# Performance work log

Measured on AMD Instinct MI355X. Metric: run time of the kernel, lower is better.

Reference implementation:

```python
import jax, jax.numpy as jnp
import numpy as np

D_K = 64

def setup_inputs() -> dict:
    key = jax.random.key(0)
    kq, kk, kv = jax.random.split(key, 3)
    B, Lq, Lk, d = 32, 2048, 2048, D_K
    return {
        "query": jax.random.normal(kq, (B, Lq, d), dtype=jnp.float32),
        "key": jax.random.normal(kk, (B, Lk, d), dtype=jnp.float32),
        "value": jax.random.normal(kv, (B, Lk, d), dtype=jnp.float32),
    }

def reference(query, key, value):
    d_k = query.shape[-1]
    scale = 1.0 / jnp.sqrt(jnp.asarray(d_k, query.dtype))
    scores = jnp.einsum('nqd,nkd->nqk', query, key) * scale  # (B, Lq, Lk)
    attn = jax.nn.softmax(scores, axis=-1)  # masked=None -> plain softmax; dropout p=0.0 is identity
    return jnp.einsum('nqk,nkd->nqd', attn, value)  # (B, Lq, d_v)
```

## Files before the change

### kernel.cpp

```cpp
#include <hip/hip_runtime.h>


#define NB   32
#define LSEQ 2048
#define DH   64
#define BM   128
#define BN   64
#define NIT  (LSEQ / BN)
#define LDP  72

typedef __attribute__((ext_vector_type(8))) __bf16 bf16x8;
typedef __attribute__((ext_vector_type(4))) float f32x4;

union BF8 { bf16x8 v; unsigned short u[8]; };

__device__ __forceinline__ unsigned short f2bf(float f) {
    unsigned int u = __builtin_bit_cast(unsigned int, f);
    u += 0x7fffu + ((u >> 16) & 1u);
    return (unsigned short)(u >> 16);
}

__device__ __forceinline__ float fast_exp2(float x) {
#if __has_builtin(__builtin_amdgcn_exp2f)
    return __builtin_amdgcn_exp2f(x);
#else
    return exp2f(x);
#endif
}

__device__ __forceinline__ void load_lds16(const void* g, void* l) {
    __builtin_amdgcn_global_load_lds(
        (const __attribute__((address_space(1))) void*)g,
        (__attribute__((address_space(3))) void*)l, 16, 0, 0);
}

__global__ __launch_bounds__(256)
void prep_k(const float* __restrict__ Kg, unsigned short* __restrict__ Kb) {
    const int CH = blockIdx.x * 256 + threadIdx.x;
    const int b   = CH >> 14;
    const int rem = CH & 16383;
    const int n   = rem >> 3;
    const int cc  = rem & 7;
    const int c   = cc ^ (n & 7);
    const float* src = Kg + (((size_t)b * LSEQ + n) * DH + c * 8);
    float4 f0 = ((const float4*)src)[0];
    float4 f1 = ((const float4*)src)[1];
    BF8 t;
    t.u[0]=f2bf(f0.x); t.u[1]=f2bf(f0.y); t.u[2]=f2bf(f0.z); t.u[3]=f2bf(f0.w);
    t.u[4]=f2bf(f1.x); t.u[5]=f2bf(f1.y); t.u[6]=f2bf(f1.z); t.u[7]=f2bf(f1.w);
    *(bf16x8*)&Kb[(size_t)CH * 8] = t.v;
}

__global__ __launch_bounds__(256)
void prep_v(const float* __restrict__ Vg, unsigned short* __restrict__ Vt) {
    __shared__ unsigned short T[64 * 65];
    const int tid = threadIdx.x;
    const int b  = blockIdx.y;
    const int nt = blockIdx.x;
    const int nl = tid >> 2;
    const int dc = (tid & 3) * 16;
    const float* src = Vg + (((size_t)b * LSEQ + nt * 64 + nl) * DH + dc);
    float4 f0 = ((const float4*)src)[0];
    float4 f1 = ((const float4*)src)[1];
    float4 f2 = ((const float4*)src)[2];
    float4 f3 = ((const float4*)src)[3];
    float vv[16] = {f0.x,f0.y,f0.z,f0.w, f1.x,f1.y,f1.z,f1.w,
                    f2.x,f2.y,f2.z,f2.w, f3.x,f3.y,f3.z,f3.w};
    #pragma unroll
    for (int i = 0; i < 16; ++i)
        T[(dc + i) * 65 + nl] = f2bf(vv[i]);
    __syncthreads();
    #pragma unroll
    for (int i = 0; i < 2; ++i) {
        const int CH = i * 256 + tid;
        const int d  = CH >> 3;
        const int cc = CH & 7;
        const int nloc = (cc ^ (d & 7)) * 8;
        BF8 o;
        #pragma unroll
        for (int j = 0; j < 8; ++j) o.u[j] = T[d * 65 + nloc + j];
        *(bf16x8*)&Vt[(((size_t)(b * 64 + d)) * 256 + nt * 8 + cc) * 8] = o.v;
    }
}

__global__ __launch_bounds__(256, 2)
void attn_fwd(const unsigned short* __restrict__ Kb,
              const unsigned short* __restrict__ Vt,
              const float* __restrict__ Qg,
              float* __restrict__ Og) {
    __shared__ __align__(16) unsigned short Klds[BN * DH];
    __shared__ __align__(16) unsigned short Vlds[DH * BN];
    __shared__ __align__(16) unsigned short Plds[4 * 32 * LDP];

    const int tid  = threadIdx.x;
    const int wave = tid >> 6;
    const int lane = tid & 63;
    const int quad = lane >> 4;
    const int l16  = lane & 15;
    const int b    = blockIdx.y;
    const int qt   = blockIdx.x;

    int fidx[4][2];
    #pragma unroll
    for (int t = 0; t < 4; ++t)
        #pragma unroll
        for (int kt = 0; kt < 2; ++kt) {
            const int n = t * 16 + l16;
            const int c = kt * 4 + quad;
            fidx[t][kt] = (n * 8 + (c ^ (n & 7))) * 8;
        }

    const float qscale = 0.18033688011112042f;
    bf16x8 qf[2][2];
    #pragma unroll
    for (int st = 0; st < 2; ++st) {
        const int row = qt * BM + wave * 32 + st * 16 + l16;
        const float* qp = Qg + (((size_t)b * LSEQ + row) * DH);
        #pragma unroll
        for (int kt = 0; kt < 2; ++kt) {
            const float* p4 = qp + kt * 32 + quad * 8;
            float4 f0 = ((const float4*)p4)[0];
            float4 f1 = ((const float4*)p4)[1];
            BF8 t;
            t.u[0]=f2bf(f0.x*qscale); t.u[1]=f2bf(f0.y*qscale);
            t.u[2]=f2bf(f0.z*qscale); t.u[3]=f2bf(f0.w*qscale);
            t.u[4]=f2bf(f1.x*qscale); t.u[5]=f2bf(f1.y*qscale);
            t.u[6]=f2bf(f1.z*qscale); t.u[7]=f2bf(f1.w*qscale);
            qf[st][kt] = t.v;
        }
    }

    f32x4 o[2][4];
    float l_run[2][4];
    #pragma unroll
    for (int st = 0; st < 2; ++st)
        #pragma unroll
        for (int t = 0; t < 4; ++t) {
            o[st][t] = (f32x4){0.f, 0.f, 0.f, 0.f};
            l_run[st][t] = 0.f;
        }

    const char* kgb = (const char*)Kb + (size_t)b * (LSEQ * DH * 2);
    const char* vgb = (const char*)Vt + (size_t)b * (DH * LSEQ * 2);
    const int L0 = wave * 128 + lane;
    const int L1 = L0 + 64;
    const int voff0 = (L0 >> 3) * (LSEQ * 2) + (L0 & 7) * 16;
    const int voff1 = (L1 >> 3) * (LSEQ * 2) + (L1 & 7) * 16;
    char* kl = (char*)Klds + wave * 2048;
    char* vl = (char*)Vlds + wave * 2048;
    unsigned short* pw = &Plds[wave * 32 * LDP];

    for (int nt = 0; nt < NIT; ++nt) {
        __syncthreads();
        load_lds16(kgb + nt * 8192 + L0 * 16, kl);
        load_lds16(kgb + nt * 8192 + L1 * 16, kl + 1024);
        load_lds16(vgb + nt * 128 + voff0, vl);
        load_lds16(vgb + nt * 128 + voff1, vl + 1024);
        __syncthreads();

        f32x4 s[2][4];
        #pragma unroll
        for (int st = 0; st < 2; ++st)
            #pragma unroll
            for (int t = 0; t < 4; ++t) s[st][t] = (f32x4){0.f, 0.f, 0.f, 0.f};
        #pragma unroll
        for (int kt = 0; kt < 2; ++kt)
            #pragma unroll
            for (int t = 0; t < 4; ++t) {
                bf16x8 kf = *(const bf16x8*)&Klds[fidx[t][kt]];
                s[0][t] = __builtin_amdgcn_mfma_f32_16x16x32_bf16(qf[0][kt], kf, s[0][t], 0, 0, 0);
                s[1][t] = __builtin_amdgcn_mfma_f32_16x16x32_bf16(qf[1][kt], kf, s[1][t], 0, 0, 0);
            }

        #pragma unroll
        for (int st = 0; st < 2; ++st)
            #pragma unroll
            for (int t = 0; t < 4; ++t)
                #pragma unroll
                for (int r = 0; r < 4; ++r) {
                    float e = fast_exp2(s[st][t][r]);
                    l_run[st][r] += e;
                    pw[(st * 16 + quad * 4 + r) * LDP + t * 16 + l16] = f2bf(e);
                }
        asm volatile("s_waitcnt lgkmcnt(0)" ::: "memory");

        #pragma unroll
        for (int kt = 0; kt < 2; ++kt) {
            bf16x8 pa0 = *(const bf16x8*)&pw[l16 * LDP + kt * 32 + quad * 8];
            bf16x8 pa1 = *(const bf16x8*)&pw[(16 + l16) * LDP + kt * 32 + quad * 8];
            #pragma unroll
            for (int t = 0; t < 4; ++t) {
                bf16x8 vf = *(const bf16x8*)&Vlds[fidx[t][kt]];
                o[0][t] = __builtin_amdgcn_mfma_f32_16x16x32_bf16(pa0, vf, o[0][t], 0, 0, 0);
                o[1][t] = __builtin_amdgcn_mfma_f32_16x16x32_bf16(pa1, vf, o[1][t], 0, 0, 0);
            }
        }
    }

    #pragma unroll
    for (int st = 0; st < 2; ++st)
        #pragma unroll
        for (int r = 0; r < 4; ++r) {
            float l = l_run[st][r];
            l += __shfl_xor(l, 1, 64);
            l += __shfl_xor(l, 2, 64);
            l += __shfl_xor(l, 4, 64);
            l += __shfl_xor(l, 8, 64);
            const float inv = 1.0f / l;
            const int row = qt * BM + wave * 32 + st * 16 + quad * 4 + r;
            float* op = Og + (((size_t)b * LSEQ + row) * DH);
            #pragma unroll
            for (int t = 0; t < 4; ++t)
                op[t * 16 + l16] = o[st][t][r] * inv;
        }
}

extern "C" void kernel_launch(void* const* d_in, const int* in_sizes, int n_in,
                              void* d_out, int out_size, void* d_ws, size_t ws_size,
                              hipStream_t stream) {
    const float* Q = (const float*)d_in[0];
    const float* K = (const float*)d_in[1];
    const float* V = (const float*)d_in[2];
    float* O = (float*)d_out;

    unsigned short* Kb = (unsigned short*)d_ws;
    unsigned short* Vt = (unsigned short*)d_ws + 4u * 1024u * 1024u;

    prep_k<<<dim3((NB * LSEQ * 8) / 256), dim3(256), 0, stream>>>(K, Kb);
    prep_v<<<dim3(LSEQ / 64, NB), dim3(256), 0, stream>>>(V, Vt);
    attn_fwd<<<dim3(LSEQ / BM, NB), dim3(256), 0, stream>>>(Kb, Vt, Q, O);
}
```

Measured before the change: 152.8 us.

## Switch attention to 32x32x16 MFMA, double-buffer K/V LDS, merge prep kernels

Replaces the 16x16x32 MFMA tiling with 32x32x16 MFMA computing S^T = K·Q^T, so each lane owns one query row and the row-sum needs only one cross-half shuffle. K/V tiles are double-buffered in LDS so the next tile's global->LDS load overlaps current compute, removing one barrier per iteration. The K and V conversion kernels are merged into one launch, and P is packed into bf16 pairs with a perm and written and read as 64-bit LDS accesses. The output is stored as float4, and the P row stride changes to 68. This uses more LDS for the double buffers and may affect occupancy. The bf16 rounding in pack_bf2 is a simplified round-half-up rather than round-to-nearest-even.

```diff
diff --git a/kernel.cpp b/kernel.cpp
--- a/kernel.cpp
+++ b/kernel.cpp
@@ -7,17 +7,23 @@
 #define BM   128
 #define BN   64
 #define NIT  (LSEQ / BN)
-#define LDP  72
-
-typedef __attribute__((ext_vector_type(8))) __bf16 bf16x8;
-typedef __attribute__((ext_vector_type(4))) float f32x4;
-
-union BF8 { bf16x8 v; unsigned short u[8]; };
+#define LDP  68
+
+typedef __attribute__((ext_vector_type(8)))  __bf16 bf16x8;
+typedef __attribute__((ext_vector_type(16))) float  f32x16;
+
+union BF8 { bf16x8 v; unsigned short u[8]; unsigned long long q[2]; };
 
 __device__ __forceinline__ unsigned short f2bf(float f) {
     unsigned int u = __builtin_bit_cast(unsigned int, f);
     u += 0x7fffu + ((u >> 16) & 1u);
     return (unsigned short)(u >> 16);
+}
+
+__device__ __forceinline__ unsigned pack_bf2(float a, float b) {
+    unsigned ua = __builtin_bit_cast(unsigned, a) + 0x8000u;
+    unsigned ub = __builtin_bit_cast(unsigned, b) + 0x8000u;
+    return __builtin_amdgcn_perm(ub, ua, 0x07060302u);
 }
 
 __device__ __forceinline__ float fast_exp2(float x) {
@@ -34,52 +40,54 @@
         (__attribute__((address_space(3))) void*)l, 16, 0, 0);
 }
 
+#define KPREP_BLOCKS ((NB * LSEQ * 8) / 256)
 __global__ __launch_bounds__(256)
-void prep_k(const float* __restrict__ Kg, unsigned short* __restrict__ Kb) {
-    const int CH = blockIdx.x * 256 + threadIdx.x;
-    const int b   = CH >> 14;
-    const int rem = CH & 16383;
-    const int n   = rem >> 3;
-    const int cc  = rem & 7;
-    const int c   = cc ^ (n & 7);
-    const float* src = Kg + (((size_t)b * LSEQ + n) * DH + c * 8);
-    float4 f0 = ((const float4*)src)[0];
-    float4 f1 = ((const float4*)src)[1];
-    BF8 t;
-    t.u[0]=f2bf(f0.x); t.u[1]=f2bf(f0.y); t.u[2]=f2bf(f0.z); t.u[3]=f2bf(f0.w);
-    t.u[4]=f2bf(f1.x); t.u[5]=f2bf(f1.y); t.u[6]=f2bf(f1.z); t.u[7]=f2bf(f1.w);
-    *(bf16x8*)&Kb[(size_t)CH * 8] = t.v;
-}
-
-__global__ __launch_bounds__(256)
-void prep_v(const float* __restrict__ Vg, unsigned short* __restrict__ Vt) {
+void prep(const float* __restrict__ Kg, const float* __restrict__ Vg,
+          unsigned short* __restrict__ Kb, unsigned short* __restrict__ Vt) {
     __shared__ unsigned short T[64 * 65];
     const int tid = threadIdx.x;
-    const int b  = blockIdx.y;
-    const int nt = blockIdx.x;
-    const int nl = tid >> 2;
-    const int dc = (tid & 3) * 16;
-    const float* src = Vg + (((size_t)b * LSEQ + nt * 64 + nl) * DH + dc);
-    float4 f0 = ((const float4*)src)[0];
-    float4 f1 = ((const float4*)src)[1];
-    float4 f2 = ((const float4*)src)[2];
-    float4 f3 = ((const float4*)src)[3];
-    float vv[16] = {f0.x,f0.y,f0.z,f0.w, f1.x,f1.y,f1.z,f1.w,
-                    f2.x,f2.y,f2.z,f2.w, f3.x,f3.y,f3.z,f3.w};
-    #pragma unroll
-    for (int i = 0; i < 16; ++i)
-        T[(dc + i) * 65 + nl] = f2bf(vv[i]);
-    __syncthreads();
-    #pragma unroll
-    for (int i = 0; i < 2; ++i) {
-        const int CH = i * 256 + tid;
-        const int d  = CH >> 3;
-        const int cc = CH & 7;
-        const int nloc = (cc ^ (d & 7)) * 8;
-        BF8 o;
-        #pragma unroll
-        for (int j = 0; j < 8; ++j) o.u[j] = T[d * 65 + nloc + j];
-        *(bf16x8*)&Vt[(((size_t)(b * 64 + d)) * 256 + nt * 8 + cc) * 8] = o.v;
+    if (blockIdx.x < KPREP_BLOCKS) {
+        const int CH  = blockIdx.x * 256 + tid;
+        const int b   = CH >> 14;
+        const int rem = CH & 16383;
+        const int n   = rem >> 3;
+        const int cc  = rem & 7;
+        const int c   = cc ^ (n & 7);
+        const float* src = Kg + (((size_t)b * LSEQ + n) * DH + c * 8);
+        float4 f0 = ((const float4*)src)[0];
+        float4 f1 = ((const float4*)src)[1];
+        BF8 t;
+        t.u[0]=f2bf(f0.x); t.u[1]=f2bf(f0.y); t.u[2]=f2bf(f0.z); t.u[3]=f2bf(f0.w);
+        t.u[4]=f2bf(f1.x); t.u[5]=f2bf(f1.y); t.u[6]=f2bf(f1.z); t.u[7]=f2bf(f1.w);
+        *(bf16x8*)&Kb[(size_t)CH * 8] = t.v;
+    } else {
+        const int bx = blockIdx.x - KPREP_BLOCKS;
+        const int b  = bx >> 5;
+        const int nt = bx & 31;
+        const int nl = tid >> 2;
+        const int dc = (tid & 3) * 16;
+        const float* src = Vg + (((size_t)b * LSEQ + nt * 64 + nl) * DH + dc);
+        float4 f0 = ((const float4*)src)[0];
+        float4 f1 = ((const float4*)src)[1];
+        float4 f2 = ((const float4*)src)[2];
+        float4 f3 = ((const float4*)src)[3];
+        float vv[16] = {f0.x,f0.y,f0.z,f0.w, f1.x,f1.y,f1.z,f1.w,
+                        f2.x,f2.y,f2.z,f2.w, f3.x,f3.y,f3.z,f3.w};
+        #pragma unroll
+        for (int i = 0; i < 16; ++i)
+            T[(dc + i) * 65 + nl] = f2bf(vv[i]);
+        __syncthreads();
+        #pragma unroll
+        for (int i = 0; i < 2; ++i) {
+            const int CH = i * 256 + tid;
+            const int d  = CH >> 3;
+            const int cc = CH & 7;
+            const int nloc = (cc ^ (d & 7)) * 8;
+            BF8 o;
+            #pragma unroll
+            for (int j = 0; j < 8; ++j) o.u[j] = T[d * 65 + nloc + j];
+            *(bf16x8*)&Vt[(((size_t)(b * 64 + d)) * 256 + nt * 8 + cc) * 8] = o.v;
+        }
     }
 }
 
@@ -88,37 +96,33 @@
               const unsigned short* __restrict__ Vt,
               const float* __restrict__ Qg,
               float* __restrict__ Og) {
-    __shared__ __align__(16) unsigned short Klds[BN * DH];
-    __shared__ __align__(16) unsigned short Vlds[DH * BN];
+    __shared__ __align__(16) unsigned short Klds[2][BN * DH];
+    __shared__ __align__(16) unsigned short Vlds[2][DH * BN];
     __shared__ __align__(16) unsigned short Plds[4 * 32 * LDP];
 
     const int tid  = threadIdx.x;
     const int wave = tid >> 6;
     const int lane = tid & 63;
-    const int quad = lane >> 4;
-    const int l16  = lane & 15;
+    const int m32  = lane & 31;
+    const int h    = lane >> 5;
     const int b    = blockIdx.y;
     const int qt   = blockIdx.x;
 
-    int fidx[4][2];
+    int fidx[2][4];
     #pragma unroll
-    for (int t = 0; t < 4; ++t)
-        #pragma unroll
-        for (int kt = 0; kt < 2; ++kt) {
-            const int n = t * 16 + l16;
-            const int c = kt * 4 + quad;
-            fidx[t][kt] = (n * 8 + (c ^ (n & 7))) * 8;
-        }
+    for (int t = 0; t < 2; ++t)
+        #pragma unroll
+        for (int kt = 0; kt < 4; ++kt)
+            fidx[t][kt] = ((t * 32 + m32) * 8 + ((kt * 2 + h) ^ (m32 & 7))) * 8;
 
     const float qscale = 0.18033688011112042f;
-    bf16x8 qf[2][2];
-    #pragma unroll
-    for (int st = 0; st < 2; ++st) {
-        const int row = qt * BM + wave * 32 + st * 16 + l16;
-        const float* qp = Qg + (((size_t)b * LSEQ + row) * DH);
-        #pragma unroll
-        for (int kt = 0; kt < 2; ++kt) {
-            const float* p4 = qp + kt * 32 + quad * 8;
+    const int qrow = qt * BM + wave * 32 + m32;
+    bf16x8 qf[4];
+    {
+        const float* qp = Qg + ((size_t)(b * LSEQ + qrow)) * DH;
+        #pragma unroll
+        for (int kt = 0; kt < 4; ++kt) {
+            const float* p4 = qp + kt * 16 + h * 8;
             float4 f0 = ((const float4*)p4)[0];
             float4 f1 = ((const float4*)p4)[1];
             BF8 t;
@@ -126,19 +130,14 @@
             t.u[2]=f2bf(f0.z*qscale); t.u[3]=f2bf(f0.w*qscale);
             t.u[4]=f2bf(f1.x*qscale); t.u[5]=f2bf(f1.y*qscale);
             t.u[6]=f2bf(f1.z*qscale); t.u[7]=f2bf(f1.w*qscale);
-            qf[st][kt] = t.v;
-        }
-    }
-
-    f32x4 o[2][4];
-    float l_run[2][4];
+            qf[kt] = t.v;
+        }
+    }
+
+    f32x16 o0, o1;
     #pragma unroll
-    for (int st = 0; st < 2; ++st)
-        #pragma unroll
-        for (int t = 0; t < 4; ++t) {
-            o[st][t] = (f32x4){0.f, 0.f, 0.f, 0.f};
-            l_run[st][t] = 0.f;
-        }
+    for (int i = 0; i < 16; ++i) { o0[i] = 0.f; o1[i] = 0.f; }
+    float l_run = 0.f;
 
     const char* kgb = (const char*)Kb + (size_t)b * (LSEQ * DH * 2);
     const char* vgb = (const char*)Vt + (size_t)b * (DH * LSEQ * 2);
@@ -146,72 +145,83 @@
     const int L1 = L0 + 64;
     const int voff0 = (L0 >> 3) * (LSEQ * 2) + (L0 & 7) * 16;
     const int voff1 = (L1 >> 3) * (LSEQ * 2) + (L1 & 7) * 16;
-    char* kl = (char*)Klds + wave * 2048;
-    char* vl = (char*)Vlds + wave * 2048;
     unsigned short* pw = &Plds[wave * 32 * LDP];
 
+    {
+        char* kl = (char*)&Klds[0][0] + wave * 2048;
+        char* vl = (char*)&Vlds[0][0] + wave * 2048;
+        load_lds16(kgb + L0 * 16, kl);
+        load_lds16(kgb + L1 * 16, kl + 1024);
+        load_lds16(vgb + voff0, vl);
+        load_lds16(vgb + voff1, vl + 1024);
+    }
+
     for (int nt = 0; nt < NIT; ++nt) {
+        const int cur = nt & 1;
         __syncthreads();
-        load_lds16(kgb + nt * 8192 + L0 * 16, kl);
-        load_lds16(kgb + nt * 8192 + L1 * 16, kl + 1024);
-        load_lds16(vgb + nt * 128 + voff0, vl);
-        load_lds16(vgb + nt * 128 + voff1, vl + 1024);
-        __syncthreads();
-
-        f32x4 s[2][4];
-        #pragma unroll
-        for (int st = 0; st < 2; ++st)
+        if (nt + 1 < NIT) {
+            char* kl = (char*)&Klds[cur ^ 1][0] + wave * 2048;
+            char* vl = (char*)&Vlds[cur ^ 1][0] + wave * 2048;
+            load_lds16(kgb + (nt + 1) * 8192 + L0 * 16, kl);
+            load_lds16(kgb + (nt + 1) * 8192 + L1 * 16, kl + 1024);
+            load_lds16(vgb + (nt + 1) * 128 + voff0, vl);
+            load_lds16(vgb + (nt + 1) * 128 + voff1, vl + 1024);
+        }
+
+        f32x16 s0, s1;
+        #pragma unroll
+        for (int i = 0; i < 16; ++i) { s0[i] = 0.f; s1[i] = 0.f; }
+        #pragma unroll
+        for (int kt = 0; kt < 4; ++kt) {
+            bf16x8 kf0 = *(const bf16x8*)&Klds[cur][fidx[0][kt]];
+            bf16x8 kf1 = *(const bf16x8*)&Klds[cur][fidx[1][kt]];
+            s0 = __builtin_amdgcn_mfma_f32_32x32x16_bf16(kf0, qf[kt], s0, 0, 0, 0);
+            s1 = __builtin_amdgcn_mfma_f32_32x32x16_bf16(kf1, qf[kt], s1, 0, 0, 0);
+        }
+
+        #pragma unroll
+        for (int t = 0; t < 2; ++t) {
             #pragma unroll
-            for (int t = 0; t < 4; ++t) s[st][t] = (f32x4){0.f, 0.f, 0.f, 0.f};
-        #pragma unroll
-        for (int kt = 0; kt < 2; ++kt)
-            #pragma unroll
-            for (int t = 0; t < 4; ++t) {
-                bf16x8 kf = *(const bf16x8*)&Klds[fidx[t][kt]];
-                s[0][t] = __builtin_amdgcn_mfma_f32_16x16x32_bf16(qf[0][kt], kf, s[0][t], 0, 0, 0);
-                s[1][t] = __builtin_amdgcn_mfma_f32_16x16x32_bf16(qf[1][kt], kf, s[1][t], 0, 0, 0);
+            for (int g = 0; g < 4; ++g) {
+                float e0 = fast_exp2(t ? s1[4*g+0] : s0[4*g+0]);
+                float e1 = fast_exp2(t ? s1[4*g+1] : s0[4*g+1]);
+                float e2 = fast_exp2(t ? s1[4*g+2] : s0[4*g+2]);
+                float e3 = fast_exp2(t ? s1[4*g+3] : s0[4*g+3]);
+                l_run += (e0 + e1) + (e2 + e3);
+                uint2 d;
+                d.x = pack_bf2(e0, e1);
+                d.y = pack_bf2(e2, e3);
+                *(uint2*)&pw[m32 * LDP + t * 32 + g * 8 + h * 4] = d;
             }
-
-        #pragma unroll
-        for (int st = 0; st < 2; ++st)
-            #pragma unroll
-            for (int t = 0; t < 4; ++t)
-                #pragma unroll
-                for (int r = 0; r < 4; ++r) {
-                    float e = fast_exp2(s[st][t][r]);
-                    l_run[st][r] += e;
-                    pw[(st * 16 + quad * 4 + r) * LDP + t * 16 + l16] = f2bf(e);
-                }
+        }
         asm volatile("s_waitcnt lgkmcnt(0)" ::: "memory");
 
         #pragma unroll
-        for (int kt = 0; kt < 2; ++kt) {
-            bf16x8 pa0 = *(const bf16x8*)&pw[l16 * LDP + kt * 32 + quad * 8];
-            bf16x8 pa1 = *(const bf16x8*)&pw[(16 + l16) * LDP + kt * 32 + quad * 8];
-            #pragma unroll
-            for (int t = 0; t < 4; ++t) {
-                bf16x8 vf = *(const bf16x8*)&Vlds[fidx[t][kt]];
-                o[0][t] = __builtin_amdgcn_mfma_f32_16x16x32_bf16(pa0, vf, o[0][t], 0, 0, 0);
-                o[1][t] = __builtin_amdgcn_mfma_f32_16x16x32_bf16(pa1, vf, o[1][t], 0, 0, 0);
-            }
-        }
-    }
-
+        for (int kt = 0; kt < 4; ++kt) {
+            BF8 pf;
+            const unsigned short* pp = &pw[m32 * LDP + kt * 16 + h * 8];
+            pf.q[0] = *(const unsigned long long*)pp;
+            pf.q[1] = *(const unsigned long long*)(pp + 4);
+            bf16x8 vf0 = *(const bf16x8*)&Vlds[cur][fidx[0][kt]];
+            bf16x8 vf1 = *(const bf16x8*)&Vlds[cur][fidx[1][kt]];
+            o0 = __builtin_amdgcn_mfma_f32_32x32x16_bf16(vf0, pf.v, o0, 0, 0, 0);
+            o1 = __builtin_amdgcn_mfma_f32_32x32x16_bf16(vf1, pf.v, o1, 0, 0, 0);
+        }
+    }
+
+    const float l = l_run + __shfl_xor(l_run, 32, 64);
+    const float inv = 1.0f / l;
+    float* op = Og + ((size_t)(b * LSEQ + qrow)) * DH;
     #pragma unroll
-    for (int st = 0; st < 2; ++st)
-        #pragma unroll
-        for (int r = 0; r < 4; ++r) {
-            float l = l_run[st][r];
-            l += __shfl_xor(l, 1, 64);
-            l += __shfl_xor(l, 2, 64);
-            l += __shfl_xor(l, 4, 64);
-            l += __shfl_xor(l, 8, 64);
-            const float inv = 1.0f / l;
-            const int row = qt * BM + wave * 32 + st * 16 + quad * 4 + r;
-            float* op = Og + (((size_t)b * LSEQ + row) * DH);
-            #pragma unroll
-            for (int t = 0; t < 4; ++t)
-                op[t * 16 + l16] = o[st][t][r] * inv;
+    for (int t = 0; t < 2; ++t)
+        #pragma unroll
+        for (int g = 0; g < 4; ++g) {
+            float4 v;
+            v.x = (t ? o1[4*g+0] : o0[4*g+0]) * inv;
+            v.y = (t ? o1[4*g+1] : o0[4*g+1]) * inv;
+            v.z = (t ? o1[4*g+2] : o0[4*g+2]) * inv;
+            v.w = (t ? o1[4*g+3] : o0[4*g+3]) * inv;
+            *(float4*)(op + t * 32 + g * 8 + h * 4) = v;
         }
 }
 
@@ -226,7 +236,6 @@
     unsigned short* Kb = (unsigned short*)d_ws;
     unsigned short* Vt = (unsigned short*)d_ws + 4u * 1024u * 1024u;
 
-    prep_k<<<dim3((NB * LSEQ * 8) / 256), dim3(256), 0, stream>>>(K, Kb);
-    prep_v<<<dim3(LSEQ / 64, NB), dim3(256), 0, stream>>>(V, Vt);
+    prep<<<dim3(KPREP_BLOCKS + NB * (LSEQ / 64)), dim3(256), 0, stream>>>(K, V, Kb, Vt);
     attn_fwd<<<dim3(LSEQ / BM, NB), dim3(256), 0, stream>>>(Kb, Vt, Q, O);
 }
```

New measurement: 145.2 us. -5.0%, faster.
